# Kernel tuning notes

Hardware: AMD Instinct MI355X
Metric: run time of the kernel (lower is better)

The kernel has to match this reference:

```python
import jax, jax.numpy as jnp
import numpy as np

N_NODES = 50000
N_EDGES = 600000
D_IN = 128
DIM = 128
N_REL = 3
N_LAYERS = 2


def setup_inputs() -> dict:
    key = jax.random.key(0)
    ks = jax.random.split(key, 10)
    s = 1.0 / np.sqrt(DIM)
    x = jax.random.normal(ks[0], (N_NODES, D_IN), dtype=jnp.float32)
    edge_index = jax.random.randint(ks[1], (2, N_EDGES), 0, N_NODES)
    edge_type = jax.random.randint(ks[2], (N_EDGES,), 0, N_REL)
    edge_weight = jax.random.uniform(ks[3], (N_EDGES,), dtype=jnp.float32)
    # stacked per-layer parameters (layer dims are uniform since D_IN == DIM)
    w_rel = jax.random.normal(ks[4], (N_LAYERS, N_REL, DIM, DIM), dtype=jnp.float32) * s
    w_root = jax.random.normal(ks[5], (N_LAYERS, DIM, DIM), dtype=jnp.float32) * s
    b_conv = jnp.zeros((N_LAYERS, DIM), dtype=jnp.float32)
    w_skip = jax.random.normal(ks[6], (N_LAYERS, D_IN, DIM), dtype=jnp.float32) * s
    b_skip = jnp.zeros((N_LAYERS, DIM), dtype=jnp.float32)
    return {"x": x, "edge_index": edge_index, "edge_type": edge_type,
            "edge_weight": edge_weight, "w_rel": w_rel, "w_root": w_root,
            "b_conv": b_conv, "w_skip": w_skip, "b_skip": b_skip}


def reference(x, edge_index, edge_type, edge_weight, w_rel, w_root, b_conv, w_skip, b_skip):
    n = x.shape[0]
    src, dst = edge_index[0], edge_index[1]
    h = x
    for l in range(w_rel.shape[0]):  # small fixed layer loop (2)
        skip = x @ w_skip[l] + b_skip[l]                      # [N, dim]
        # per-relation transform of all nodes: [R, N, dim] (cheap GEMMs),
        # avoids materializing a per-edge [E, d, d] weight gather
        hr = jnp.einsum('nd,rde->rne', h, w_rel[l])
        msgs = hr[edge_type, src] * edge_weight[:, None]      # [E, dim] gather
        agg = jax.ops.segment_sum(msgs, dst, num_segments=n)  # scatter-add
        h = agg + h @ w_root[l] + b_conv[l] + skip            # conv + skip residual
    return h
```

## Files before the change

### kernel.cpp

```cpp
#include <hip/hip_runtime.h>


#define DIM 128

typedef short short8 __attribute__((ext_vector_type(8)));
typedef float f32x4 __attribute__((ext_vector_type(4)));

__device__ __forceinline__ unsigned short f2bf(float f) {
    unsigned u = __float_as_uint(f);
    unsigned r = (u + 0x7FFFu + ((u >> 16) & 1u)) >> 16;
    return (unsigned short)r;
}
__device__ __forceinline__ float bflo(unsigned p) { return __uint_as_float(p << 16); }
__device__ __forceinline__ float bfhi(unsigned p) { return __uint_as_float(p & 0xFFFF0000u); }

__global__ void zero_kernel(int4* __restrict__ p, int n4) {
    int i = blockIdx.x * 256 + threadIdx.x;
    if (i < n4) p[i] = make_int4(0, 0, 0, 0);
}

#define K2_CONVB 2048
#define K2_PREPB 256
#define K2_CNTB  512

__device__ void conv_body(const float* __restrict__ in, unsigned short* __restrict__ ob,
                          int n8, int bid) {
    for (int i = bid * 256 + threadIdx.x; i < n8; i += K2_CONVB * 256) {
        const float4* ip = reinterpret_cast<const float4*>(in) + (size_t)i * 2;
        float4 v0 = ip[0], v1 = ip[1];
        uint4 o;
        o.x = (unsigned)f2bf(v0.x) | ((unsigned)f2bf(v0.y) << 16);
        o.y = (unsigned)f2bf(v0.z) | ((unsigned)f2bf(v0.w) << 16);
        o.z = (unsigned)f2bf(v1.x) | ((unsigned)f2bf(v1.y) << 16);
        o.w = (unsigned)f2bf(v1.z) | ((unsigned)f2bf(v1.w) << 16);
        reinterpret_cast<uint4*>(ob)[i] = o;
    }
}

__device__ void prep_body(const float* __restrict__ w_rel, const float* __restrict__ w_root,
                          const float* __restrict__ w_skip, unsigned short* __restrict__ WTf,
                          int bid) {
    for (int i = bid * 256 + threadIdx.x; i < 2 * 5 * DIM * DIM; i += K2_PREPB * 256) {
        int j    = i & 7;
        int lane = (i >> 3) & 63;
        int ks   = (i >> 9) & 3;
        int n    = (i >> 11) & 7;
        int s    = (i >> 14) % 5;
        int l    = i / (5 * DIM * DIM);
        int col = n * 16 + (lane & 15);
        int k   = ks * 32 + (lane >> 4) * 8 + j;
        float v;
        if (s < 3)       v = w_rel[(((size_t)l * 3 + s) * DIM + k) * DIM + col];
        else if (s == 3) {
            v = w_root[((size_t)l * DIM + k) * DIM + col];
            if (l == 0) v += w_skip[((size_t)k) * DIM + col];
        } else           v = w_skip[((size_t)l * DIM + k) * DIM + col];
        WTf[i] = f2bf(v);
    }
}

__device__ void count_body(const int* __restrict__ dst, int* __restrict__ counts,
                           unsigned short* __restrict__ rank, int E, int bid) {
    for (int i = bid * 256 + threadIdx.x; i < E; i += K2_CNTB * 256) {
        int r = atomicAdd(&counts[dst[i]], 1);
        rank[i] = (unsigned short)r;
    }
}

__global__ __launch_bounds__(256) void fat_prep(
    const float* __restrict__ x, unsigned short* __restrict__ xb, int n8,
    const float* __restrict__ w_rel, const float* __restrict__ w_root,
    const float* __restrict__ w_skip, unsigned short* __restrict__ WTf,
    const int* __restrict__ dst, int* __restrict__ counts,
    unsigned short* __restrict__ rank, int E) {
    int b = blockIdx.x;
    if (b < K2_CONVB)                 conv_body(x, xb, n8, b);
    else if (b < K2_CONVB + K2_PREPB) prep_body(w_rel, w_root, w_skip, WTf, b - K2_CONVB);
    else                              count_body(dst, counts, rank, E, b - K2_CONVB - K2_PREPB);
}

__global__ void bsum_kernel(const int* __restrict__ counts, int* __restrict__ bsums, int n) {
    int t = threadIdx.x;
    int i = blockIdx.x * 256 + t;
    int v = (i < n) ? counts[i] : 0;
    for (int d = 32; d; d >>= 1) v += __shfl_down(v, d);
    __shared__ int ws[4];
    if ((t & 63) == 0) ws[t >> 6] = v;
    __syncthreads();
    if (t == 0) bsums[blockIdx.x] = ws[0] + ws[1] + ws[2] + ws[3];
}

__global__ void bscan_kernel(const int* __restrict__ bsums, int* __restrict__ bpre, int nblk) {
    __shared__ int s[256];
    int t = threadIdx.x;
    int v = (t < nblk) ? bsums[t] : 0;
    s[t] = v;
    __syncthreads();
    for (int d = 1; d < 256; d <<= 1) {
        int u = (t >= d) ? s[t - d] : 0;
        __syncthreads();
        s[t] += u;
        __syncthreads();
    }
    bpre[t] = s[t] - v;
}

__global__ void scan_final(const int* __restrict__ counts, const int* __restrict__ bpre,
                           int* __restrict__ offsets, int n, int E) {
    __shared__ int s[256];
    int t = threadIdx.x;
    int i = blockIdx.x * 256 + t;
    int v = (i < n) ? counts[i] : 0;
    s[t] = v;
    __syncthreads();
    for (int d = 1; d < 256; d <<= 1) {
        int u = (t >= d) ? s[t - d] : 0;
        __syncthreads();
        s[t] += u;
        __syncthreads();
    }
    int ex = s[t] - v + bpre[blockIdx.x];
    if (i < n) offsets[i] = ex;
    if (i == 0) offsets[n] = E;
}

template<bool HAS_SKIP>
__device__ void gemm_body(
    int bid,
    const unsigned short* __restrict__ Ab, const unsigned short* __restrict__ Xb,
    const unsigned short* __restrict__ WTf,
    const float* __restrict__ bconv, const float* __restrict__ bskip,
    unsigned short* __restrict__ hr, void* __restrict__ outp, int M) {
    constexpr int NF = HAS_SKIP ? 40 : 32;
    int t = threadIdx.x, lane = t & 63, wid = t >> 6;
    int lrow = lane & 15, lhi = lane >> 4;
    int r0 = bid * 128 + wid * 32;

    short8 af[2][4];
    #pragma unroll
    for (int rg = 0; rg < 2; ++rg) {
        int r = r0 + rg * 16 + lrow;
        const unsigned short* ap = Ab + (size_t)(r < M ? r : 0) * DIM + lhi * 8;
        #pragma unroll
        for (int ks = 0; ks < 4; ++ks)
            af[rg][ks] = *reinterpret_cast<const short8*>(ap + ks * 32);
    }
    short8 xf[2][4];
    f32x4 acc34[2][8];

    short8 b0[4], b1[4];
    auto loadB = [&](int fi, short8* bb) {
        const unsigned short* p = WTf + ((size_t)fi * 4 * 64 + lane) * 8;
        #pragma unroll
        for (int ks = 0; ks < 4; ++ks)
            bb[ks] = *reinterpret_cast<const short8*>(p + ks * 512);
    };
    loadB(0, b0);
    #pragma unroll
    for (int fi = 0; fi < NF; ++fi) {
        short8* bc = (fi & 1) ? b1 : b0;
        short8* bn = (fi & 1) ? b0 : b1;
        if (fi + 1 < NF) loadB(fi + 1, bn);
        const int slot = fi >> 3, n = fi & 7;
        const int col = n * 16 + lrow;
        if (HAS_SKIP && slot == 3 && n == 0) {
            #pragma unroll
            for (int rg = 0; rg < 2; ++rg) {
                int r = r0 + rg * 16 + lrow;
                const unsigned short* xp = Xb + (size_t)(r < M ? r : 0) * DIM + lhi * 8;
                #pragma unroll
                for (int ks = 0; ks < 4; ++ks)
                    xf[rg][ks] = *reinterpret_cast<const short8*>(xp + ks * 32);
            }
        }
        if (slot < 3) {
            f32x4 a0 = {0.f, 0.f, 0.f, 0.f}, a1 = {0.f, 0.f, 0.f, 0.f};
            #pragma unroll
            for (int ks = 0; ks < 4; ++ks) {
                a0 = __builtin_amdgcn_mfma_f32_16x16x32_bf16(af[0][ks], bc[ks], a0, 0, 0, 0);
                a1 = __builtin_amdgcn_mfma_f32_16x16x32_bf16(af[1][ks], bc[ks], a1, 0, 0, 0);
            }
            unsigned short* hp = hr + (size_t)slot * M * DIM;
            #pragma unroll
            for (int rg = 0; rg < 2; ++rg) {
                f32x4& aa = rg ? a1 : a0;
                #pragma unroll
                for (int i2 = 0; i2 < 4; ++i2) {
                    int r = r0 + rg * 16 + lhi * 4 + i2;
                    if (r < M) hp[(size_t)r * DIM + col] = f2bf(aa[i2]);
                }
            }
        } else if (!HAS_SKIP) {
            f32x4 a0 = {0.f, 0.f, 0.f, 0.f}, a1 = {0.f, 0.f, 0.f, 0.f};
            #pragma unroll
            for (int ks = 0; ks < 4; ++ks) {
                a0 = __builtin_amdgcn_mfma_f32_16x16x32_bf16(af[0][ks], bc[ks], a0, 0, 0, 0);
                a1 = __builtin_amdgcn_mfma_f32_16x16x32_bf16(af[1][ks], bc[ks], a1, 0, 0, 0);
            }
            float bb = bconv[col] + bskip[col];
            unsigned short* op = (unsigned short*)outp;
            #pragma unroll
            for (int rg = 0; rg < 2; ++rg) {
                f32x4& aa = rg ? a1 : a0;
                #pragma unroll
                for (int i2 = 0; i2 < 4; ++i2) {
                    int r = r0 + rg * 16 + lhi * 4 + i2;
                    if (r < M) op[(size_t)r * DIM + col] = f2bf(aa[i2] + bb);
                }
            }
        } else if (slot == 3) {
            f32x4 z = {0.f, 0.f, 0.f, 0.f};
            acc34[0][n] = z; acc34[1][n] = z;
            #pragma unroll
            for (int ks = 0; ks < 4; ++ks) {
                acc34[0][n] = __builtin_amdgcn_mfma_f32_16x16x32_bf16(af[0][ks], bc[ks], acc34[0][n], 0, 0, 0);
                acc34[1][n] = __builtin_amdgcn_mfma_f32_16x16x32_bf16(af[1][ks], bc[ks], acc34[1][n], 0, 0, 0);
            }
        } else {
            #pragma unroll
            for (int ks = 0; ks < 4; ++ks) {
                acc34[0][n] = __builtin_amdgcn_mfma_f32_16x16x32_bf16(xf[0][ks], bc[ks], acc34[0][n], 0, 0, 0);
                acc34[1][n] = __builtin_amdgcn_mfma_f32_16x16x32_bf16(xf[1][ks], bc[ks], acc34[1][n], 0, 0, 0);
            }
            float bb = bconv[col] + bskip[col];
            float* op = (float*)outp;
            #pragma unroll
            for (int rg = 0; rg < 2; ++rg) {
                #pragma unroll
                for (int i2 = 0; i2 < 4; ++i2) {
                    int r = r0 + rg * 16 + lhi * 4 + i2;
                    if (r < M) op[(size_t)r * DIM + col] = acc34[rg][n][i2] + bb;
                }
            }
        }
    }
}

#define K6_SCTB 512

__device__ void scatter_body(const int* __restrict__ src, const int* __restrict__ dst,
                             const int* __restrict__ etype, const float* __restrict__ ew,
                             const int* __restrict__ offsets,
                             const unsigned short* __restrict__ rank,
                             unsigned* __restrict__ csr, int E, int bid) {
    for (int i = bid * 256 + threadIdx.x; i < E; i += K6_SCTB * 256) {
        int d = dst[i];
        int p = offsets[d] + rank[i];
        unsigned wq = (unsigned)__float2uint_rn(ew[i] * 16383.0f);
        csr[p] = (unsigned)src[i] | ((unsigned)etype[i] << 16) | (wq << 18);
    }
}

__global__ __launch_bounds__(256) void gemm0_scatter(
    const unsigned short* __restrict__ Ab, const unsigned short* __restrict__ WTf,
    const float* __restrict__ bconv, const float* __restrict__ bskip,
    unsigned short* __restrict__ hr, unsigned short* __restrict__ h1, int M, int GB,
    const int* __restrict__ src, const int* __restrict__ dst,
    const int* __restrict__ etype, const float* __restrict__ ew,
    const int* __restrict__ offsets, const unsigned short* __restrict__ rank,
    unsigned* __restrict__ csr, int E) {
    int b = blockIdx.x;
    if (b < GB) gemm_body<false>(b, Ab, nullptr, WTf, bconv, bskip, hr, h1, M);
    else        scatter_body(src, dst, etype, ew, offsets, rank, csr, E, b - GB);
}

__global__ __launch_bounds__(256) void gemm1_kernel(
    const unsigned short* __restrict__ Ab, const unsigned short* __restrict__ Xb,
    const unsigned short* __restrict__ WTf,
    const float* __restrict__ bconv, const float* __restrict__ bskip,
    unsigned short* __restrict__ hr, float* __restrict__ outp, int M) {
    gemm_body<true>(blockIdx.x, Ab, Xb, WTf, bconv, bskip, hr, outp, M);
}

template<bool BF16IO>
__global__ __launch_bounds__(256) void agg_kernel(
    const unsigned short* __restrict__ hr, const unsigned* __restrict__ csr,
    const int* __restrict__ offsets, float* __restrict__ outf,
    unsigned short* __restrict__ outb, int N) {
    int t = threadIdx.x;
    int lane = t & 63;
    int v = blockIdx.x * 4 + (t >> 6);
    if (v >= N) return;
    int g = lane >> 4;
    int l16 = lane & 15;
    int beg = offsets[v], end = offsets[v + 1];

    float acc[8] = {0.f, 0.f, 0.f, 0.f, 0.f, 0.f, 0.f, 0.f};
    int i = beg + g;
    bool valid = i < end;
    unsigned st = valid ? csr[i] : 0u;
    while (__any(valid)) {
        int ni = i + 4;
        bool nv = ni < end;
        unsigned nst = nv ? csr[ni] : 0u;
        if (valid) {
            int srcn = st & 0xFFFF;
            int rel  = (st >> 16) & 3;
            float w  = (float)(st >> 18) * (1.0f / 16383.0f);
            const unsigned short* row = hr + ((size_t)rel * N + srcn) * DIM + l16 * 8;
            uint4 pv = *reinterpret_cast<const uint4*>(row);
            acc[0] += w * bflo(pv.x); acc[1] += w * bfhi(pv.x);
            acc[2] += w * bflo(pv.y); acc[3] += w * bfhi(pv.y);
            acc[4] += w * bflo(pv.z); acc[5] += w * bfhi(pv.z);
            acc[6] += w * bflo(pv.w); acc[7] += w * bfhi(pv.w);
        }
        i = ni; st = nst; valid = nv;
    }
    #pragma unroll
    for (int j = 0; j < 8; ++j) {
        acc[j] += __shfl_xor(acc[j], 16);
        acc[j] += __shfl_xor(acc[j], 32);
    }
    if (g == 0) {
        if (BF16IO) {
            unsigned short* op = outb + (size_t)v * DIM + l16 * 8;
            uint4 cur = *reinterpret_cast<const uint4*>(op);
            float r0 = bflo(cur.x) + acc[0], r1 = bfhi(cur.x) + acc[1];
            float r2 = bflo(cur.y) + acc[2], r3 = bfhi(cur.y) + acc[3];
            float r4 = bflo(cur.z) + acc[4], r5 = bfhi(cur.z) + acc[5];
            float r6 = bflo(cur.w) + acc[6], r7 = bfhi(cur.w) + acc[7];
            uint4 o;
            o.x = (unsigned)f2bf(r0) | ((unsigned)f2bf(r1) << 16);
            o.y = (unsigned)f2bf(r2) | ((unsigned)f2bf(r3) << 16);
            o.z = (unsigned)f2bf(r4) | ((unsigned)f2bf(r5) << 16);
            o.w = (unsigned)f2bf(r6) | ((unsigned)f2bf(r7) << 16);
            *reinterpret_cast<uint4*>(op) = o;
        } else {
            float* op = outf + (size_t)v * DIM + l16 * 8;
            float4 c0 = *reinterpret_cast<float4*>(op);
            float4 c1 = *reinterpret_cast<float4*>(op + 4);
            c0.x += acc[0]; c0.y += acc[1]; c0.z += acc[2]; c0.w += acc[3];
            c1.x += acc[4]; c1.y += acc[5]; c1.z += acc[6]; c1.w += acc[7];
            *reinterpret_cast<float4*>(op) = c0;
            *reinterpret_cast<float4*>(op + 4) = c1;
        }
    }
}

extern "C" void kernel_launch(void* const* d_in, const int* in_sizes, int n_in,
                              void* d_out, int out_size, void* d_ws, size_t ws_size,
                              hipStream_t stream) {
    const float* x       = (const float*)d_in[0];
    const int*   eidx    = (const int*)d_in[1];
    const int*   etype   = (const int*)d_in[2];
    const float* ew      = (const float*)d_in[3];
    const float* w_rel   = (const float*)d_in[4];
    const float* w_root  = (const float*)d_in[5];
    const float* b_conv  = (const float*)d_in[6];
    const float* w_skip  = (const float*)d_in[7];
    const float* b_skip  = (const float*)d_in[8];

    const int N = in_sizes[0] / DIM;
    const int E = in_sizes[3];
    const int* src = eidx;
    const int* dst = eidx + E;
    const int nblk = (N + 255) / 256;

    char* w = (char*)d_ws;
    unsigned short* WTf  = (unsigned short*)w;  w += (size_t)2 * 5 * DIM * DIM * 2;
    unsigned short* xb   = (unsigned short*)w;  w += (size_t)N * DIM * 2;
    unsigned short* hr   = (unsigned short*)w;  w += (size_t)3 * N * DIM * 2;
    unsigned short* h1   = (unsigned short*)w;  w += (size_t)N * DIM * 2;
    int* counts          = (int*)w;             w += (size_t)N * 4;
    int* offsets         = (int*)w;             w += (size_t)(N + 4) * 4;
    int* bsums           = (int*)w;             w += (size_t)256 * 4;
    int* bpre            = (int*)w;             w += (size_t)256 * 4;
    unsigned short* rank = (unsigned short*)w;  w += (size_t)E * 2;
    unsigned* csr        = (unsigned*)w;        w += (size_t)E * 4;

    float* out = (float*)d_out;

    const int n8 = N * DIM / 8;
    zero_kernel<<<(N / 4 + 255) / 256, 256, 0, stream>>>((int4*)counts, N / 4);
    fat_prep<<<K2_CONVB + K2_PREPB + K2_CNTB, 256, 0, stream>>>(
        x, xb, n8, w_rel, w_root, w_skip, WTf, dst, counts, rank, E);
    bsum_kernel<<<nblk, 256, 0, stream>>>(counts, bsums, N);
    bscan_kernel<<<1, 256, 0, stream>>>(bsums, bpre, nblk);
    scan_final<<<nblk, 256, 0, stream>>>(counts, bpre, offsets, N, E);

    int GB = (N + 127) / 128;
    int ablocks = (N + 3) / 4;
    gemm0_scatter<<<GB + K6_SCTB, 256, 0, stream>>>(
        xb, WTf, b_conv, b_skip, hr, h1, N, GB,
        src, dst, etype, ew, offsets, rank, csr, E);
    agg_kernel<true><<<ablocks, 256, 0, stream>>>(hr, csr, offsets, nullptr, h1, N);
    gemm1_kernel<<<GB, 256, 0, stream>>>(h1, xb, WTf + (size_t)5 * DIM * DIM,
                                         b_conv + DIM, b_skip + DIM, hr, out, N);
    agg_kernel<false><<<ablocks, 256, 0, stream>>>(hr, csr, offsets, out, nullptr, N);
}
```

Measured before the change: 171.1 us.

## Shrink GEMM row tile, deepen weight prefetch, prefetch gathered rows in aggregation

The GEMM tile shrinks from 32 to 16 rows per wave (64 rows per block), which doubles the number of blocks and cuts register use for more occupancy. The weight-fragment prefetch goes from double to triple buffering. The aggregation loop now software-pipelines the gather of the next hr row, so the load of edge i+4 is in flight while edge i is accumulated. The cost is that weight fragments get reloaded more often per row across the extra blocks.

```diff
diff --git a/kernel.cpp b/kernel.cpp
--- a/kernel.cpp
+++ b/kernel.cpp
@@ -134,103 +134,80 @@
     constexpr int NF = HAS_SKIP ? 40 : 32;
     int t = threadIdx.x, lane = t & 63, wid = t >> 6;
     int lrow = lane & 15, lhi = lane >> 4;
-    int r0 = bid * 128 + wid * 32;
-
-    short8 af[2][4];
-    #pragma unroll
-    for (int rg = 0; rg < 2; ++rg) {
-        int r = r0 + rg * 16 + lrow;
+    int r0 = bid * 64 + wid * 16;
+
+    short8 af[4];
+    {
+        int r = r0 + lrow;
         const unsigned short* ap = Ab + (size_t)(r < M ? r : 0) * DIM + lhi * 8;
         #pragma unroll
         for (int ks = 0; ks < 4; ++ks)
-            af[rg][ks] = *reinterpret_cast<const short8*>(ap + ks * 32);
-    }
-    short8 xf[2][4];
-    f32x4 acc34[2][8];
-
-    short8 b0[4], b1[4];
-    auto loadB = [&](int fi, short8* bb) {
+            af[ks] = *reinterpret_cast<const short8*>(ap + ks * 32);
+    }
+    short8 xf[4];
+    f32x4 acc34[8];
+
+    short8 bb[3][4];
+    auto loadB = [&](int fi, short8* dstb) {
         const unsigned short* p = WTf + ((size_t)fi * 4 * 64 + lane) * 8;
         #pragma unroll
         for (int ks = 0; ks < 4; ++ks)
-            bb[ks] = *reinterpret_cast<const short8*>(p + ks * 512);
+            dstb[ks] = *reinterpret_cast<const short8*>(p + ks * 512);
     };
-    loadB(0, b0);
+    loadB(0, bb[0]);
+    loadB(1, bb[1]);
     #pragma unroll
     for (int fi = 0; fi < NF; ++fi) {
-        short8* bc = (fi & 1) ? b1 : b0;
-        short8* bn = (fi & 1) ? b0 : b1;
-        if (fi + 1 < NF) loadB(fi + 1, bn);
+        short8* bc = bb[fi % 3];
+        if (fi + 2 < NF) loadB(fi + 2, bb[(fi + 2) % 3]);
         const int slot = fi >> 3, n = fi & 7;
         const int col = n * 16 + lrow;
         if (HAS_SKIP && slot == 3 && n == 0) {
-            #pragma unroll
-            for (int rg = 0; rg < 2; ++rg) {
-                int r = r0 + rg * 16 + lrow;
-                const unsigned short* xp = Xb + (size_t)(r < M ? r : 0) * DIM + lhi * 8;
-                #pragma unroll
-                for (int ks = 0; ks < 4; ++ks)
-                    xf[rg][ks] = *reinterpret_cast<const short8*>(xp + ks * 32);
-            }
+            int r = r0 + lrow;
+            const unsigned short* xp = Xb + (size_t)(r < M ? r : 0) * DIM + lhi * 8;
+            #pragma unroll
+            for (int ks = 0; ks < 4; ++ks)
+                xf[ks] = *reinterpret_cast<const short8*>(xp + ks * 32);
         }
         if (slot < 3) {
-            f32x4 a0 = {0.f, 0.f, 0.f, 0.f}, a1 = {0.f, 0.f, 0.f, 0.f};
-            #pragma unroll
-            for (int ks = 0; ks < 4; ++ks) {
-                a0 = __builtin_amdgcn_mfma_f32_16x16x32_bf16(af[0][ks], bc[ks], a0, 0, 0, 0);
-                a1 = __builtin_amdgcn_mfma_f32_16x16x32_bf16(af[1][ks], bc[ks], a1, 0, 0, 0);
-            }
+            f32x4 a0 = {0.f, 0.f, 0.f, 0.f};
+            #pragma unroll
+            for (int ks = 0; ks < 4; ++ks)
+                a0 = __builtin_amdgcn_mfma_f32_16x16x32_bf16(af[ks], bc[ks], a0, 0, 0, 0);
             unsigned short* hp = hr + (size_t)slot * M * DIM;
             #pragma unroll
-            for (int rg = 0; rg < 2; ++rg) {
-                f32x4& aa = rg ? a1 : a0;
-                #pragma unroll
-                for (int i2 = 0; i2 < 4; ++i2) {
-                    int r = r0 + rg * 16 + lhi * 4 + i2;
-                    if (r < M) hp[(size_t)r * DIM + col] = f2bf(aa[i2]);
-                }
+            for (int i2 = 0; i2 < 4; ++i2) {
+                int r = r0 + lhi * 4 + i2;
+                if (r < M) hp[(size_t)r * DIM + col] = f2bf(a0[i2]);
             }
         } else if (!HAS_SKIP) {
-            f32x4 a0 = {0.f, 0.f, 0.f, 0.f}, a1 = {0.f, 0.f, 0.f, 0.f};
-            #pragma unroll
-            for (int ks = 0; ks < 4; ++ks) {
-                a0 = __builtin_amdgcn_mfma_f32_16x16x32_bf16(af[0][ks], bc[ks], a0, 0, 0, 0);
-                a1 = __builtin_amdgcn_mfma_f32_16x16x32_bf16(af[1][ks], bc[ks], a1, 0, 0, 0);
-            }
-            float bb = bconv[col] + bskip[col];
+            f32x4 a0 = {0.f, 0.f, 0.f, 0.f};
+            #pragma unroll
+            for (int ks = 0; ks < 4; ++ks)
+                a0 = __builtin_amdgcn_mfma_f32_16x16x32_bf16(af[ks], bc[ks], a0, 0, 0, 0);
+            float bbias = bconv[col] + bskip[col];
             unsigned short* op = (unsigned short*)outp;
             #pragma unroll
-            for (int rg = 0; rg < 2; ++rg) {
-                f32x4& aa = rg ? a1 : a0;
-                #pragma unroll
-                for (int i2 = 0; i2 < 4; ++i2) {
-                    int r = r0 + rg * 16 + lhi * 4 + i2;
-                    if (r < M) op[(size_t)r * DIM + col] = f2bf(aa[i2] + bb);
-                }
+            for (int i2 = 0; i2 < 4; ++i2) {
+                int r = r0 + lhi * 4 + i2;
+                if (r < M) op[(size_t)r * DIM + col] = f2bf(a0[i2] + bbias);
             }
         } else if (slot == 3) {
             f32x4 z = {0.f, 0.f, 0.f, 0.f};
-            acc34[0][n] = z; acc34[1][n] = z;
-            #pragma unroll
-            for (int ks = 0; ks < 4; ++ks) {
-                acc34[0][n] = __builtin_amdgcn_mfma_f32_16x16x32_bf16(af[0][ks], bc[ks], acc34[0][n], 0, 0, 0);
-                acc34[1][n] = __builtin_amdgcn_mfma_f32_16x16x32_bf16(af[1][ks], bc[ks], acc34[1][n], 0, 0, 0);
-            }
+            acc34[n] = z;
+            #pragma unroll
+            for (int ks = 0; ks < 4; ++ks)
+                acc34[n] = __builtin_amdgcn_mfma_f32_16x16x32_bf16(af[ks], bc[ks], acc34[n], 0, 0, 0);
         } else {
             #pragma unroll
-            for (int ks = 0; ks < 4; ++ks) {
-                acc34[0][n] = __builtin_amdgcn_mfma_f32_16x16x32_bf16(xf[0][ks], bc[ks], acc34[0][n], 0, 0, 0);
-                acc34[1][n] = __builtin_amdgcn_mfma_f32_16x16x32_bf16(xf[1][ks], bc[ks], acc34[1][n], 0, 0, 0);
-            }
-            float bb = bconv[col] + bskip[col];
+            for (int ks = 0; ks < 4; ++ks)
+                acc34[n] = __builtin_amdgcn_mfma_f32_16x16x32_bf16(xf[ks], bc[ks], acc34[n], 0, 0, 0);
+            float bbias = bconv[col] + bskip[col];
             float* op = (float*)outp;
             #pragma unroll
-            for (int rg = 0; rg < 2; ++rg) {
-                #pragma unroll
-                for (int i2 = 0; i2 < 4; ++i2) {
-                    int r = r0 + rg * 16 + lhi * 4 + i2;
-                    if (r < M) op[(size_t)r * DIM + col] = acc34[rg][n][i2] + bb;
-                }
+            for (int i2 = 0; i2 < 4; ++i2) {
+                int r = r0 + lhi * 4 + i2;
+                if (r < M) op[(size_t)r * DIM + col] = acc34[n][i2] + bbias;
             }
         }
     }
@@ -287,24 +264,30 @@
 
     float acc[8] = {0.f, 0.f, 0.f, 0.f, 0.f, 0.f, 0.f, 0.f};
     int i = beg + g;
-    bool valid = i < end;
-    unsigned st = valid ? csr[i] : 0u;
-    while (__any(valid)) {
-        int ni = i + 4;
-        bool nv = ni < end;
-        unsigned nst = nv ? csr[ni] : 0u;
-        if (valid) {
-            int srcn = st & 0xFFFF;
-            int rel  = (st >> 16) & 3;
-            float w  = (float)(st >> 18) * (1.0f / 16383.0f);
-            const unsigned short* row = hr + ((size_t)rel * N + srcn) * DIM + l16 * 8;
-            uint4 pv = *reinterpret_cast<const uint4*>(row);
-            acc[0] += w * bflo(pv.x); acc[1] += w * bfhi(pv.x);
-            acc[2] += w * bflo(pv.y); acc[3] += w * bfhi(pv.y);
-            acc[4] += w * bflo(pv.z); acc[5] += w * bfhi(pv.z);
-            acc[6] += w * bflo(pv.w); acc[7] += w * bfhi(pv.w);
-        }
-        i = ni; st = nst; valid = nv;
+    bool v0 = i < end;
+    unsigned st0 = v0 ? csr[i] : 0u;
+    uint4 pv0 = make_uint4(0, 0, 0, 0);
+    if (v0) {
+        const unsigned short* row = hr + ((size_t)((st0 >> 16) & 3) * N + (st0 & 0xFFFF)) * DIM + l16 * 8;
+        pv0 = *reinterpret_cast<const uint4*>(row);
+    }
+    while (__any(v0)) {
+        int i1 = i + 4;
+        bool v1 = i1 < end;
+        unsigned st1 = v1 ? csr[i1] : 0u;
+        uint4 pv1 = make_uint4(0, 0, 0, 0);
+        if (v1) {
+            const unsigned short* row = hr + ((size_t)((st1 >> 16) & 3) * N + (st1 & 0xFFFF)) * DIM + l16 * 8;
+            pv1 = *reinterpret_cast<const uint4*>(row);
+        }
+        if (v0) {
+            float w = (float)(st0 >> 18) * (1.0f / 16383.0f);
+            acc[0] += w * bflo(pv0.x); acc[1] += w * bfhi(pv0.x);
+            acc[2] += w * bflo(pv0.y); acc[3] += w * bfhi(pv0.y);
+            acc[4] += w * bflo(pv0.z); acc[5] += w * bfhi(pv0.z);
+            acc[6] += w * bflo(pv0.w); acc[7] += w * bfhi(pv0.w);
+        }
+        i = i1; st0 = st1; pv0 = pv1; v0 = v1;
     }
     #pragma unroll
     for (int j = 0; j < 8; ++j) {
@@ -378,7 +361,7 @@
     bscan_kernel<<<1, 256, 0, stream>>>(bsums, bpre, nblk);
     scan_final<<<nblk, 256, 0, stream>>>(counts, bpre, offsets, N, E);
 
-    int GB = (N + 127) / 128;
+    int GB = (N + 63) / 64;
     int ablocks = (N + 3) / 4;
     gemm0_scatter<<<GB + K6_SCTB, 256, 0, stream>>>(
         xb, WTf, b_conv, b_skip, hr, h1, N, GB,
```

After: 182.3 us. 1.07x slower.
